# Kernel tuning notes

Measured on AMD Instinct MI355X. Metric: run time of the kernel, lower is better.

## Reference

```python
import jax, jax.numpy as jnp
import numpy as np

M_BITS = 4            # mem_pot_bits
M_MASK = (1 << M_BITS) - 1
T_MASK = (1 << 4) - 1  # t_bits = 4
ALPHA = 0.5


def setup_inputs() -> dict:
    key = jax.random.key(0)
    ks = jax.random.split(key, 8)
    B, N_IN, N_OUT, M = 256, 4096, 4096, 1 << M_BITS
    return {
        "active_mask": jax.random.randint(ks[0], (B, N_IN), 0, 2, dtype=jnp.int32),
        "t": 7,
        "prev_neuron_id": jax.random.randint(ks[1], (N_IN,), 0, M, dtype=jnp.int32),
        "t_last": jnp.zeros((B,), jnp.int32),
        "mem_fict": jax.random.uniform(ks[2], (B, N_OUT), jnp.float32),
        "mem_phys": jax.random.randint(ks[3], (B, N_OUT), 0, M, dtype=jnp.int32),
        "accumulate_lut_delta": jnp.zeros((N_OUT, M), jnp.float32),
        "tau": jax.random.uniform(ks[4], (N_OUT,), jnp.float32),
        "v_th": jax.random.uniform(ks[5], (N_OUT,), jnp.float32),
        "syn_w": jax.random.uniform(ks[6], (N_IN, N_OUT), jnp.float32),
        "mem_map": jax.nn.sigmoid(jax.random.normal(ks[7], (N_OUT, M), jnp.float32)),
    }


def reference(active_mask, t, prev_neuron_id, t_last, mem_fict, mem_phys,
              accumulate_lut_delta, tau, v_th, syn_w, mem_map):
    # delta_t = (t - t_last) & t_bit_mask  (Python '&' binds looser than '-')
    delta_t = (t - t_last) & T_MASK                          # (B,)
    t_last_new = jnp.full_like(t_last, t)

    # masked matmul + exponential membrane decay
    weights_sum = active_mask.astype(jnp.float32) @ syn_w    # (B, N_out)
    decay = jnp.exp(-tau[None, :] * delta_t[:, None].astype(jnp.float32))
    mem_fict_new = mem_fict * decay + weights_sum

    # XOR tree-reduction over masked input ids == bitwise parity per bit.
    # Only the low M_BITS matter (result is masked by m_bit_mask afterwards).
    masked_ids = jnp.where(active_mask.astype(bool), prev_neuron_id[None, :], 0)
    shifts = jnp.arange(M_BITS, dtype=jnp.int32)
    bits = (masked_ids[:, :, None] >> shifts) & 1            # (B, N_in, M_BITS)
    parity = jnp.sum(bits, axis=1) & 1                       # (B, M_BITS)
    acc = jnp.sum(parity << shifts, axis=1)                  # (B,)

    # physical membrane update (all low-bit integer ops)
    mem_phys_new = (mem_phys ^ delta_t[:, None] ^ acc[:, None]) & M_MASK

    # LUT gather + threshold
    n_out = mem_map.shape[0]
    rows = jnp.broadcast_to(jnp.arange(n_out)[None, :], mem_phys_new.shape)
    v_map_vals = mem_map[rows, mem_phys_new]                 # (B, N_out)
    active_next = v_map_vals >= v_th[None, :]

    # scatter-add per-bucket LUT delta (alpha != 0 path)
    delta = ALPHA * (mem_phys_new.astype(jnp.float32) - v_map_vals)
    lut_new = accumulate_lut_delta.at[rows, mem_phys_new].add(delta)

    return active_next, mem_fict_new, mem_phys_new, lut_new, t_last_new
```

## Files before the change

### kernel.cpp

```cpp
#include <hip/hip_runtime.h>

typedef __attribute__((ext_vector_type(8))) short short8;
typedef __attribute__((ext_vector_type(4))) float f32x4;
typedef unsigned int u32;

#define N_IN  4096
#define N_OUT 4096
#define NBAT  256

#define OUT_ACT   0
#define OUT_FICT  1048576
#define OUT_PHYS  2097152
#define OUT_LUT   3145728
#define OUT_TLAST 3211264

#define WS_MASK   0
#define WS_PART   2097152
#define WS_DTF    (WS_PART + 16777216)
#define WS_DXA    (WS_DTF + 1024)

#define BM 128
#define BN 32
#define BK 64
#define SPLITK 4
#define KCHUNK (N_IN / SPLITK)
#define NTK (KCHUNK / BK)

__device__ __forceinline__ unsigned f2bf(float f) {
  unsigned u = __float_as_uint(f);
  return (u + 0x7FFFu + ((u >> 16) & 1u)) >> 16;
}

__device__ __forceinline__ void gload16(const void* g, void* l) {
  __builtin_amdgcn_global_load_lds(
      (const __attribute__((address_space(1))) u32*)g,
      (__attribute__((address_space(3))) u32*)l, 16, 0, 0);
}

__global__ __launch_bounds__(256) void snn_pre(
    const int* __restrict__ mask, const int* __restrict__ t_ptr,
    const int* __restrict__ pid, const int* __restrict__ t_last,
    float* __restrict__ dtf_ws, int* __restrict__ dxa_ws,
    u32* __restrict__ maskws, float* __restrict__ out)
{
  const int b = blockIdx.x, tid = threadIdx.x;
  const int k0 = tid * 16;
  const int4* mp = (const int4*)(mask + (size_t)b * N_IN + k0);
  const int4* pp = (const int4*)(pid + k0);
  int x = 0;
  u32 wv[8];
#pragma unroll
  for (int q = 0; q < 4; ++q) {
    int4 m = mp[q];
    int4 id = pp[q];
    x ^= (m.x ? id.x : 0) ^ (m.y ? id.y : 0) ^ (m.z ? id.z : 0) ^ (m.w ? id.w : 0);
    wv[q * 2]     = (m.x ? 0x3F80u : 0u) | ((m.y ? 0x3F80u : 0u) << 16);
    wv[q * 2 + 1] = (m.z ? 0x3F80u : 0u) | ((m.w ? 0x3F80u : 0u) << 16);
  }
  {
    const int kt = tid >> 2;
    const int gg = (tid & 3) * 2;
    u32* base = maskws + (size_t)b * 2048 + kt * 32;
    int g0 = gg ^ (b & 7), g1 = (gg + 1) ^ (b & 7);
    uint4 v0; v0.x = wv[0]; v0.y = wv[1]; v0.z = wv[2]; v0.w = wv[3];
    uint4 v1; v1.x = wv[4]; v1.y = wv[5]; v1.z = wv[6]; v1.w = wv[7];
    *(uint4*)(base + g0 * 4) = v0;
    *(uint4*)(base + g1 * 4) = v1;
  }
  x ^= __shfl_xor(x, 32); x ^= __shfl_xor(x, 16); x ^= __shfl_xor(x, 8);
  x ^= __shfl_xor(x, 4);  x ^= __shfl_xor(x, 2);  x ^= __shfl_xor(x, 1);
  __shared__ int wx[4];
  if ((tid & 63) == 0) wx[tid >> 6] = x;
  __syncthreads();
  if (tid == 0) {
    int acc = wx[0] ^ wx[1] ^ wx[2] ^ wx[3];
    int tt = t_ptr[0];
    int dt = (tt - t_last[b]) & 15;
    dtf_ws[b] = (float)dt;
    dxa_ws[b] = dt ^ (acc & 15);
    out[OUT_TLAST + b] = (float)tt;
  }
}

__global__ __launch_bounds__(256) void snn_gemm(
    const char* __restrict__ maskws, const float* __restrict__ synw,
    float* __restrict__ part)
{
  __shared__ __align__(16) char ldsA[2][BM * BK * 2];
  __shared__ __align__(16) char ldsB[2][BN * BK * 2];

  const int tid = threadIdx.x;
  const int lane = tid & 63, wid = tid >> 6;
  const int l15 = lane & 15, l4 = lane >> 4;

  const int bid = blockIdx.x;
  const int sid = (bid & 7) * 128 + (bid >> 3);
  const int nb = sid >> 3;
  const int mb = (sid >> 2) & 1;
  const int kc = sid & 3;
  const int bmb = mb * BM, bnb = nb * BN, kcb = kc * KCHUNK;

  const char* a_gbase = maskws + (size_t)bmb * 8192 + (size_t)kcb * 2;
  const int b_n = tid & 31;
  const int b_ko = tid >> 5;
  const float* b_gbase = synw + (size_t)(kcb + b_ko * 8) * N_OUT + bnb + b_n;

  auto issueA = [&](int kt) {
    char* dbase = &ldsA[kt & 1][wid * 1024];
    const char* g0 = a_gbase + (size_t)(tid >> 3) * 8192 + kt * 128 + (tid & 7) * 16;
#pragma unroll
    for (int i = 0; i < 4; ++i)
      gload16(g0 + (size_t)i * (32 * 8192), dbase + i * 4096);
  };
  auto loadB = [&](int kt, float* bv) {
    const float* g = b_gbase + (size_t)kt * BK * N_OUT;
#pragma unroll
    for (int j = 0; j < 8; ++j) bv[j] = g[(size_t)j * N_OUT];
  };
  auto writeB = [&](const float* bv, int buf) {
    u32 w[4];
#pragma unroll
    for (int p = 0; p < 4; ++p) w[p] = f2bf(bv[2 * p]) | (f2bf(bv[2 * p + 1]) << 16);
    uint4 v; v.x = w[0]; v.y = w[1]; v.z = w[2]; v.w = w[3];
    *(uint4*)(&ldsB[buf][b_n * 128 + ((b_ko ^ (b_n & 7)) * 16)]) = v;
  };

  f32x4 acc[2][2] = {};

  auto compute = [&](int buf) {
#pragma unroll
    for (int kk = 0; kk < 2; ++kk) {
      const int g0 = kk * 4 + l4;
      short8 a[2], b[2];
#pragma unroll
      for (int mi = 0; mi < 2; ++mi) {
        int row = wid * 32 + mi * 16 + l15;
        a[mi] = *(const short8*)(&ldsA[buf][row * 128 + ((g0 ^ (row & 7)) * 16)]);
      }
#pragma unroll
      for (int nj = 0; nj < 2; ++nj) {
        int col = nj * 16 + l15;
        b[nj] = *(const short8*)(&ldsB[buf][col * 128 + ((g0 ^ (col & 7)) * 16)]);
      }
#pragma unroll
      for (int mi = 0; mi < 2; ++mi)
#pragma unroll
        for (int nj = 0; nj < 2; ++nj)
          acc[mi][nj] = __builtin_amdgcn_mfma_f32_16x16x32_bf16(a[mi], b[nj], acc[mi][nj], 0, 0, 0);
    }
  };

  float bvA[8], bvB[8];

  issueA(0);
  loadB(0, bvA);
  loadB(1, bvB);

#define BODY(KT, CURBV)                                            \
  {                                                                \
    writeB(CURBV, (KT) & 1);                                       \
    loadB(((KT) + 2) & 15, CURBV);                                 \
    __builtin_amdgcn_sched_barrier(0);                             \
    asm volatile("s_waitcnt vmcnt(8) lgkmcnt(0)" ::: "memory");    \
    __builtin_amdgcn_s_barrier();                                  \
    __builtin_amdgcn_sched_barrier(0);                             \
    issueA(((KT) + 1) & 15);                                       \
    compute((KT) & 1);                                             \
  }

  for (int kt = 0; kt < NTK; kt += 2) {
    BODY(kt, bvA);
    BODY(kt + 1, bvB);
  }
#undef BODY

  float* pb = part + (size_t)kc * (NBAT * N_OUT);
#pragma unroll
  for (int mi = 0; mi < 2; ++mi)
#pragma unroll
    for (int nj = 0; nj < 2; ++nj) {
      const int o = bnb + nj * 16 + l15;
#pragma unroll
      for (int r = 0; r < 4; ++r) {
        const int b = bmb + wid * 32 + mi * 16 + l4 * 4 + r;
        pb[(size_t)b * N_OUT + o] = acc[mi][nj][r];
      }
    }
}

__global__ __launch_bounds__(256) void snn_reduce(
    const float* __restrict__ part, const float* __restrict__ memf,
    const int* __restrict__ memp, const float* __restrict__ tau,
    const float* __restrict__ vth, const float* __restrict__ mem_map,
    const float* __restrict__ dtf_ws, const int* __restrict__ dxa_ws,
    float* __restrict__ out)
{
  const int flat = (blockIdx.x * 256 + threadIdx.x) * 4;
  const int b = flat >> 12, o = flat & 4095;
  const float4 p0 = *(const float4*)(part + flat);
  const float4 p1 = *(const float4*)(part + 1048576 + flat);
  const float4 p2 = *(const float4*)(part + 2097152 + flat);
  const float4 p3 = *(const float4*)(part + 3145728 + flat);
  float4 ws;
  ws.x = (p0.x + p1.x) + (p2.x + p3.x);
  ws.y = (p0.y + p1.y) + (p2.y + p3.y);
  ws.z = (p0.z + p1.z) + (p2.z + p3.z);
  ws.w = (p0.w + p1.w) + (p2.w + p3.w);
  const float dtf = dtf_ws[b];
  const int dxa = dxa_ws[b];
  const float4 mf = *(const float4*)(memf + flat);
  const int4  mp = *(const int4*)(memp + flat);
  const float4 tv = *(const float4*)(tau + o);
  const float4 vv = *(const float4*)(vth + o);
  float4 act, fict, phys;
#define DO(c, oi) { float d = __expf(-tv.c * dtf); fict.c = mf.c * d + ws.c; \
                    int mpn = (mp.c ^ dxa) & 15; phys.c = (float)mpn; \
                    act.c = (mem_map[(o + oi) * 16 + mpn] >= vv.c) ? 1.f : 0.f; }
  DO(x, 0) DO(y, 1) DO(z, 2) DO(w, 3)
#undef DO
  *(float4*)(out + OUT_ACT  + flat) = act;
  *(float4*)(out + OUT_FICT + flat) = fict;
  *(float4*)(out + OUT_PHYS + flat) = phys;
}

__global__ __launch_bounds__(256) void snn_lut(
    const int* __restrict__ memp, const int* __restrict__ dxa_ws,
    const float* __restrict__ mem_map, const float* __restrict__ lut_in,
    float* __restrict__ out)
{
  __shared__ int mp[NBAT * 16];
  __shared__ int dxs[NBAT];
  const int tid = threadIdx.x;
  const int o0 = blockIdx.x * 16;
#pragma unroll
  for (int i = 0; i < 16; ++i) {
    int b = i * 16 + (tid >> 4);
    int oj = tid & 15;
    mp[b * 16 + oj] = memp[(size_t)b * N_OUT + o0 + oj];
  }
  dxs[tid] = dxa_ws[tid];
  __syncthreads();
  const int o_l = tid >> 4, m = tid & 15;
  int cnt = 0;
#pragma unroll 8
  for (int b = 0; b < NBAT; ++b) {
    int v = (mp[b * 16 + o_l] ^ dxs[b]) & 15;
    cnt += (v == m);
  }
  const int o = o0 + o_l;
  const float vmap = mem_map[o * 16 + m];
  out[OUT_LUT + o * 16 + m] = lut_in[o * 16 + m] + 0.5f * ((float)m - vmap) * (float)cnt;
}

extern "C" void kernel_launch(void* const* d_in, const int* in_sizes, int n_in,
                              void* d_out, int out_size, void* d_ws, size_t ws_size,
                              hipStream_t stream)
{
  const int*   mask    = (const int*)d_in[0];
  const int*   t_ptr   = (const int*)d_in[1];
  const int*   pid     = (const int*)d_in[2];
  const int*   t_last  = (const int*)d_in[3];
  const float* memf    = (const float*)d_in[4];
  const int*   memp    = (const int*)d_in[5];
  const float* lut_in  = (const float*)d_in[6];
  const float* tau     = (const float*)d_in[7];
  const float* vth     = (const float*)d_in[8];
  const float* synw    = (const float*)d_in[9];
  const float* mem_map = (const float*)d_in[10];
  float* out = (float*)d_out;

  char* wsb = (char*)d_ws;
  u32*   maskws = (u32*)(wsb + WS_MASK);
  float* part   = (float*)(wsb + WS_PART);
  float* dtf_ws = (float*)(wsb + WS_DTF);
  int*   dxa_ws = (int*)(wsb + WS_DXA);

  snn_pre<<<NBAT, 256, 0, stream>>>(mask, t_ptr, pid, t_last, dtf_ws, dxa_ws, maskws, out);
  snn_gemm<<<(NBAT / BM) * (N_OUT / BN) * SPLITK, 256, 0, stream>>>(
      (const char*)maskws, synw, part);
  snn_reduce<<<(NBAT * N_OUT) / 1024, 256, 0, stream>>>(
      part, memf, memp, tau, vth, mem_map, dtf_ws, dxa_ws, out);
  snn_lut<<<NBAT, 256, 0, stream>>>(memp, dxa_ws, mem_map, lut_in, out);
}
```

Baseline: 48.20 us.

## Pre-swizzle mask into MFMA fragment layout and load A directly to registers

The pre-pass now writes the bf16 activation mask in per-lane MFMA fragment order, so the GEMM loads A operands straight into registers with coalesced 16-byte loads and drops the A tile from LDS and the global-to-LDS path. The B loads switch to float4 vector loads with a new LDS packing, and the pipeline is restructured with register double-buffering for A. This removes LDS traffic and bank pressure for A but raises register use and relies on the exact fragment mapping being correct.

```diff
diff --git a/kernel.cpp b/kernel.cpp
--- a/kernel.cpp
+++ b/kernel.cpp
@@ -14,7 +14,7 @@
 #define OUT_LUT   3145728
 #define OUT_TLAST 3211264
 
-#define WS_MASK   0
+#define WS_AIMG   0
 #define WS_PART   2097152
 #define WS_DTF    (WS_PART + 16777216)
 #define WS_DXA    (WS_DTF + 1024)
@@ -31,17 +31,11 @@
   return (u + 0x7FFFu + ((u >> 16) & 1u)) >> 16;
 }
 
-__device__ __forceinline__ void gload16(const void* g, void* l) {
-  __builtin_amdgcn_global_load_lds(
-      (const __attribute__((address_space(1))) u32*)g,
-      (__attribute__((address_space(3))) u32*)l, 16, 0, 0);
-}
-
 __global__ __launch_bounds__(256) void snn_pre(
     const int* __restrict__ mask, const int* __restrict__ t_ptr,
     const int* __restrict__ pid, const int* __restrict__ t_last,
     float* __restrict__ dtf_ws, int* __restrict__ dxa_ws,
-    u32* __restrict__ maskws, float* __restrict__ out)
+    char* __restrict__ aimg, float* __restrict__ out)
 {
   const int b = blockIdx.x, tid = threadIdx.x;
   const int k0 = tid * 16;
@@ -58,14 +52,14 @@
     wv[q * 2 + 1] = (m.z ? 0x3F80u : 0u) | ((m.w ? 0x3F80u : 0u) << 16);
   }
   {
-    const int kt = tid >> 2;
-    const int gg = (tid & 3) * 2;
-    u32* base = maskws + (size_t)b * 2048 + kt * 32;
-    int g0 = gg ^ (b & 7), g1 = (gg + 1) ^ (b & 7);
+    const int rg = b >> 5, rl = b & 31;
+    const int mi = rl >> 4, l15 = rl & 15;
+    const int ktg = tid >> 2, kk = (tid >> 1) & 1, l4_0 = (tid & 1) * 2;
+    char* base = aimg + ((size_t)((rg * 64 + ktg) * 4 + kk * 2 + mi) << 10);
     uint4 v0; v0.x = wv[0]; v0.y = wv[1]; v0.z = wv[2]; v0.w = wv[3];
     uint4 v1; v1.x = wv[4]; v1.y = wv[5]; v1.z = wv[6]; v1.w = wv[7];
-    *(uint4*)(base + g0 * 4) = v0;
-    *(uint4*)(base + g1 * 4) = v1;
+    *(uint4*)(base + (l4_0 * 16 + l15) * 16)       = v0;
+    *(uint4*)(base + ((l4_0 + 1) * 16 + l15) * 16) = v1;
   }
   x ^= __shfl_xor(x, 32); x ^= __shfl_xor(x, 16); x ^= __shfl_xor(x, 8);
   x ^= __shfl_xor(x, 4);  x ^= __shfl_xor(x, 2);  x ^= __shfl_xor(x, 1);
@@ -83,10 +77,9 @@
 }
 
 __global__ __launch_bounds__(256) void snn_gemm(
-    const char* __restrict__ maskws, const float* __restrict__ synw,
+    const char* __restrict__ aimg, const float* __restrict__ synw,
     float* __restrict__ part)
 {
-  __shared__ __align__(16) char ldsA[2][BM * BK * 2];
   __shared__ __align__(16) char ldsB[2][BN * BK * 2];
 
   const int tid = threadIdx.x;
@@ -99,48 +92,49 @@
   const int mb = (sid >> 2) & 1;
   const int kc = sid & 3;
   const int bmb = mb * BM, bnb = nb * BN, kcb = kc * KCHUNK;
-
-  const char* a_gbase = maskws + (size_t)bmb * 8192 + (size_t)kcb * 2;
-  const int b_n = tid & 31;
-  const int b_ko = tid >> 5;
-  const float* b_gbase = synw + (size_t)(kcb + b_ko * 8) * N_OUT + bnb + b_n;
-
-  auto issueA = [&](int kt) {
-    char* dbase = &ldsA[kt & 1][wid * 1024];
-    const char* g0 = a_gbase + (size_t)(tid >> 3) * 8192 + kt * 128 + (tid & 7) * 16;
-#pragma unroll
-    for (int i = 0; i < 4; ++i)
-      gload16(g0 + (size_t)i * (32 * 8192), dbase + i * 4096);
-  };
-  auto loadB = [&](int kt, float* bv) {
-    const float* g = b_gbase + (size_t)kt * BK * N_OUT;
-#pragma unroll
-    for (int j = 0; j < 8; ++j) bv[j] = g[(size_t)j * N_OUT];
-  };
-  auto writeB = [&](const float* bv, int buf) {
-    u32 w[4];
-#pragma unroll
-    for (int p = 0; p < 4; ++p) w[p] = f2bf(bv[2 * p]) | (f2bf(bv[2 * p + 1]) << 16);
-    uint4 v; v.x = w[0]; v.y = w[1]; v.z = w[2]; v.w = w[3];
-    *(uint4*)(&ldsB[buf][b_n * 128 + ((b_ko ^ (b_n & 7)) * 16)]) = v;
+  const int rg = mb * 4 + wid;
+
+  const char* a_base = aimg + (((size_t)(rg * 64 + kc * 16) * 4) << 10) + lane * 16;
+
+  const int b_rr = (tid & 31) * 2;
+  const int b_n0 = (tid >> 5) * 4;
+  const float* b_base = synw + ((size_t)(kcb + b_rr) << 12) + bnb + b_n0;
+
+  auto loadA = [&](int t, uint4* d) {
+    const char* p = a_base + ((size_t)t << 12);
+#pragma unroll
+    for (int f = 0; f < 4; ++f) d[f] = *(const uint4*)(p + (f << 10));
+  };
+  auto loadB = [&](int t, float4* d) {
+    const float* p = b_base + ((size_t)t << 18);
+    d[0] = *(const float4*)(p);
+    d[1] = *(const float4*)(p + 4096);
+  };
+  auto writeB = [&](const float4* v, int buf) {
+    const float* r0 = (const float*)&v[0];
+    const float* r1 = (const float*)&v[1];
+#pragma unroll
+    for (int i = 0; i < 4; ++i) {
+      int n = b_n0 + i;
+      u32 pk = f2bf(r0[i]) | (f2bf(r1[i]) << 16);
+      *(u32*)(&ldsB[buf][n * 128 + (((b_rr >> 3) ^ (n & 7)) << 4) + ((b_rr & 7) << 1)]) = pk;
+    }
   };
 
   f32x4 acc[2][2] = {};
 
-  auto compute = [&](int buf) {
+  auto compute = [&](int buf, const uint4* af) {
 #pragma unroll
     for (int kk = 0; kk < 2; ++kk) {
       const int g0 = kk * 4 + l4;
       short8 a[2], b[2];
 #pragma unroll
-      for (int mi = 0; mi < 2; ++mi) {
-        int row = wid * 32 + mi * 16 + l15;
-        a[mi] = *(const short8*)(&ldsA[buf][row * 128 + ((g0 ^ (row & 7)) * 16)]);
-      }
+      for (int mi = 0; mi < 2; ++mi)
+        a[mi] = *(const short8*)&af[kk * 2 + mi];
 #pragma unroll
       for (int nj = 0; nj < 2; ++nj) {
         int col = nj * 16 + l15;
-        b[nj] = *(const short8*)(&ldsB[buf][col * 128 + ((g0 ^ (col & 7)) * 16)]);
+        b[nj] = *(const short8*)(&ldsB[buf][col * 128 + ((g0 ^ (col & 7)) << 4)]);
       }
 #pragma unroll
       for (int mi = 0; mi < 2; ++mi)
@@ -150,29 +144,28 @@
     }
   };
 
-  float bvA[8], bvB[8];
-
-  issueA(0);
-  loadB(0, bvA);
-  loadB(1, bvB);
-
-#define BODY(KT, CURBV)                                            \
-  {                                                                \
-    writeB(CURBV, (KT) & 1);                                       \
-    loadB(((KT) + 2) & 15, CURBV);                                 \
-    __builtin_amdgcn_sched_barrier(0);                             \
-    asm volatile("s_waitcnt vmcnt(8) lgkmcnt(0)" ::: "memory");    \
-    __builtin_amdgcn_s_barrier();                                  \
-    __builtin_amdgcn_sched_barrier(0);                             \
-    issueA(((KT) + 1) & 15);                                       \
-    compute((KT) & 1);                                             \
-  }
-
-  for (int kt = 0; kt < NTK; kt += 2) {
-    BODY(kt, bvA);
-    BODY(kt + 1, bvB);
-  }
-#undef BODY
+  uint4  aA[4], aB[4];
+  float4 bA[2], bB[2];
+
+  loadB(0, bA); loadA(0, aA);
+  loadB(1, bB); loadA(1, aB);
+
+#define PHASE(T, BV, AV, BUF)                                 \
+  {                                                           \
+    writeB(BV, BUF);                                          \
+    if ((T) + 2 < NTK) loadB((T) + 2, BV);                    \
+    asm volatile("s_waitcnt lgkmcnt(0)" ::: "memory");        \
+    __builtin_amdgcn_s_barrier();                             \
+    __builtin_amdgcn_sched_barrier(0);                        \
+    compute(BUF, AV);                                         \
+    if ((T) + 2 < NTK) loadA((T) + 2, AV);                    \
+  }
+
+  for (int t = 0; t < NTK; t += 2) {
+    PHASE(t,     bA, aA, 0)
+    PHASE(t + 1, bB, aB, 1)
+  }
+#undef PHASE
 
   float* pb = part + (size_t)kc * (NBAT * N_OUT);
 #pragma unroll
@@ -270,14 +263,14 @@
   float* out = (float*)d_out;
 
   char* wsb = (char*)d_ws;
-  u32*   maskws = (u32*)(wsb + WS_MASK);
+  char*  aimg   = wsb + WS_AIMG;
   float* part   = (float*)(wsb + WS_PART);
   float* dtf_ws = (float*)(wsb + WS_DTF);
   int*   dxa_ws = (int*)(wsb + WS_DXA);
 
-  snn_pre<<<NBAT, 256, 0, stream>>>(mask, t_ptr, pid, t_last, dtf_ws, dxa_ws, maskws, out);
+  snn_pre<<<NBAT, 256, 0, stream>>>(mask, t_ptr, pid, t_last, dtf_ws, dxa_ws, aimg, out);
   snn_gemm<<<(NBAT / BM) * (N_OUT / BN) * SPLITK, 256, 0, stream>>>(
-      (const char*)maskws, synw, part);
+      aimg, synw, part);
   snn_reduce<<<(NBAT * N_OUT) / 1024, 256, 0, stream>>>(
       part, memf, memp, tau, vth, mem_map, dtf_ws, dxa_ws, out);
   snn_lut<<<NBAT, 256, 0, stream>>>(memp, dxa_ws, mem_map, lut_in, out);
```

Measured after the change: 55.19 us. +14.5%, slower.
